# Performance work log

Measured on AMD Instinct MI355X. Metric: run time of the kernel, lower is better.

The kernel has to match this reference:

```python
import jax, jax.numpy as jnp
import numpy as np

D_MODEL = 512
NHEAD = 8
HEAD_DIM = D_MODEL // NHEAD  # 64, also rotary_dim
WIN_LO, WIN_HI = 127, 128    # attn_window: kv in [q-127, q+128]
BLOCK = 256                  # block size for banded attention (>= WIN_LO+1 and >= WIN_HI)


def setup_inputs() -> dict:
    key = jax.random.key(0)
    k1, k2, k3, k4 = jax.random.split(key, 4)
    N, T = 4, 2048
    x = jax.random.normal(k1, (N, T, D_MODEL), dtype=jnp.float32)
    Wqkv_w = jax.random.normal(k2, (3 * D_MODEL, D_MODEL), dtype=jnp.float32) * 0.02
    out_w = jax.random.normal(k3, (D_MODEL, D_MODEL), dtype=jnp.float32) * 0.02
    out_b = jax.random.normal(k4, (D_MODEL,), dtype=jnp.float32) * 0.02
    return {"x": x, "Wqkv_w": Wqkv_w, "out_w": out_w, "out_b": out_b}


def _rotate_half(u):
    u1, u2 = jnp.split(u, 2, axis=-1)
    return jnp.concatenate((-u2, u1), axis=-1)


def _apply_rope(q, k, T, dtype):
    # inv_freq: [HEAD_DIM/2]
    inv_freq = 1.0 / (10000.0 ** (jnp.arange(0, HEAD_DIM, 2, dtype=jnp.float32) / HEAD_DIM))
    pos = jnp.arange(T, dtype=dtype)
    freqs = pos[:, None] * inv_freq[None, :].astype(dtype)      # [T, D/2]
    emb = jnp.concatenate((freqs, freqs), axis=-1)              # [T, D]
    cos = jnp.cos(emb)[None, :, None, :]                        # [1,T,1,D]
    sin = jnp.sin(emb)[None, :, None, :]
    q = q * cos + _rotate_half(q) * sin
    k = k * cos + _rotate_half(k) * sin
    return q, k


def reference(x, Wqkv_w, out_w, out_b):
    N, T, dm = x.shape
    H, D, B = NHEAD, HEAD_DIM, BLOCK
    qkv = (x @ Wqkv_w.T).reshape(N, T, 3, H, D)
    q, k, v = qkv[:, :, 0], qkv[:, :, 1], qkv[:, :, 2]          # [N,T,H,D]
    q, k = _apply_rope(q, k, T, x.dtype)
    # [N,H,T,D]
    q = q.transpose(0, 2, 1, 3)
    k = k.transpose(0, 2, 1, 3)
    v = v.transpose(0, 2, 1, 3)

    nb = T // B
    qb = q.reshape(N, H, nb, B, D)
    kb = k.reshape(N, H, nb, B, D)
    vb = v.reshape(N, H, nb, B, D)
    # pad one block of zeros on each side so block g sees key blocks g-1,g,g+1
    pad = ((0, 0), (0, 0), (1, 1), (0, 0), (0, 0))
    kp = jnp.pad(kb, pad)
    vp = jnp.pad(vb, pad)
    # [N,H,nb,3B,D]
    kwin = jnp.concatenate([kp[:, :, i:i + nb] for i in range(3)], axis=3)
    vwin = jnp.concatenate([vp[:, :, i:i + nb] for i in range(3)], axis=3)

    scale = 1.0 / np.sqrt(D)
    scores = jnp.einsum('nhgqd,nhgkd->nhgqk', qb, kwin) * scale  # [N,H,nb,B,3B]

    qi = jnp.arange(B)
    kj = jnp.arange(3 * B)
    gidx = jnp.arange(nb)
    diff = kj[None, None, :] - B - qi[None, :, None]             # [1,B,3B] kv - q offset
    band = (diff >= -WIN_LO) & (diff <= WIN_HI)
    kv_global = gidx[:, None, None] * B + kj[None, None, :] - B  # [nb,1,3B]
    valid = (kv_global >= 0) & (kv_global < T)
    mask = band & valid                                          # [nb,B,3B]

    neg = jnp.asarray(-1e30, dtype=scores.dtype)
    scores = jnp.where(mask[None, None], scores, neg)
    probs = jax.nn.softmax(scores, axis=-1)
    attn = jnp.einsum('nhgqk,nhgkd->nhgqd', probs, vwin)         # [N,H,nb,B,D]
    attn = attn.reshape(N, H, T, D).transpose(0, 2, 1, 3).reshape(N, T, dm)
    return attn @ out_w.T + out_b
```

## Files before the change

kernel.cpp:

```cpp
#include <hip/hip_runtime.h>
#include <math.h>


typedef __attribute__((ext_vector_type(8))) __bf16 bf16x8;
typedef __attribute__((ext_vector_type(4))) float f32x4;

__device__ __forceinline__ unsigned short f2bf(float f) {
    unsigned int u = __float_as_uint(f);
    u += 0x7fffu + ((u >> 16) & 1u);
    return (unsigned short)(u >> 16);
}
__device__ __forceinline__ unsigned int packbf2(float a, float b) {
    unsigned int ua = __float_as_uint(a); ua += 0x7fffu + ((ua >> 16) & 1u);
    unsigned int ub = __float_as_uint(b); ub += 0x7fffu + ((ub >> 16) & 1u);
    return (ua >> 16) | (ub & 0xffff0000u);
}
__device__ __forceinline__ bf16x8 as_bf16x8(uint4 u) {
    union { uint4 u4; bf16x8 v; } c; c.u4 = u; return c.v;
}
__device__ __forceinline__ bf16x8 ld_frag(const unsigned short* p) {
    return as_bf16x8(*(const uint4*)p);
}

__device__ __forceinline__ void async16(void* lds, const void* g) {
    __builtin_amdgcn_global_load_lds(
        (const __attribute__((address_space(1))) void*)g,
        (__attribute__((address_space(3))) void*)lds,
        16, 0, 0);
}

__global__ __launch_bounds__(256) void cvt_all(
    const float* __restrict__ x, const float* __restrict__ w1,
    const float* __restrict__ w2,
    unsigned short* __restrict__ xb, unsigned short* __restrict__ w1b,
    unsigned short* __restrict__ w2b)
{
    const int n_x  = 8192 * 512 / 4;
    const int n_w1 = 1536 * 512 / 4;
    const int n_w2 = 512 * 512 / 4;
    int i = blockIdx.x * 256 + threadIdx.x;
    const float* in; unsigned short* out; int j;
    if (i < n_x)                    { in = x;  out = xb;  j = i; }
    else if (i < n_x + n_w1)        { in = w1; out = w1b; j = i - n_x; }
    else if (i < n_x + n_w1 + n_w2) { in = w2; out = w2b; j = i - n_x - n_w1; }
    else return;
    float4 v = *(const float4*)(in + 4 * (size_t)j);
    uint2 o;
    o.x = packbf2(v.x, v.y);
    o.y = packbf2(v.z, v.w);
    *(uint2*)(out + 4 * (size_t)j) = o;
}

__global__ __launch_bounds__(256) void gemm_bt_mfma(
    const unsigned short* __restrict__ A, const unsigned short* __restrict__ B,
    const float* __restrict__ bias, void* __restrict__ Cout,
    int M, int O, int K, int write_bf16, int do_rope)
{
    __shared__ __align__(16) unsigned short As[128 * 64];
    __shared__ __align__(16) unsigned short Bs[64 * 64];

    const int tid  = threadIdx.x;
    const int wave = tid >> 6;
    const int lane = tid & 63;
    const int l15  = lane & 15;
    const int lg   = lane >> 4;
    const int row0 = blockIdx.x * 128;
    const int col0 = blockIdx.y * 64;
    const int wr   = wave * 32;

    f32x4 acc[2][4] = {};

    const int srow = tid >> 3;
    const int skg  = ((tid & 7) * 8) ^ ((srow & 7) * 8);

    const int fx = (l15 & 7) * 8;

    for (int k0 = 0; k0 < K; k0 += 64) {
        #pragma unroll
        for (int s = 0; s < 4; ++s)
            async16(&As[(size_t)(s * 256 + tid) * 8],
                    A + (size_t)(row0 + s * 32 + srow) * K + k0 + skg);
        #pragma unroll
        for (int s = 0; s < 2; ++s)
            async16(&Bs[(size_t)(s * 256 + tid) * 8],
                    B + (size_t)(col0 + s * 32 + srow) * K + k0 + skg);
        __syncthreads();

        #pragma unroll
        for (int kstep = 0; kstep < 2; ++kstep) {
            const int kq = (kstep * 32 + lg * 8) ^ fx;
            bf16x8 af[2], bfr[4];
            #pragma unroll
            for (int mt = 0; mt < 2; ++mt)
                af[mt] = ld_frag(&As[(wr + mt * 16 + l15) * 64 + kq]);
            #pragma unroll
            for (int nt = 0; nt < 4; ++nt)
                bfr[nt] = ld_frag(&Bs[(nt * 16 + l15) * 64 + kq]);
            #pragma unroll
            for (int mt = 0; mt < 2; ++mt)
                #pragma unroll
                for (int nt = 0; nt < 4; ++nt)
                    acc[mt][nt] = __builtin_amdgcn_mfma_f32_16x16x32_bf16(
                        af[mt], bfr[nt], acc[mt][nt], 0, 0, 0);
        }
        __syncthreads();
    }

    const int qrow = lg * 4;

    if (do_rope && col0 < 1024) {
        const float cfreq = 0.28782313662425574f;
        const float invf0 = __expf(-(float)l15 * cfreq);
        const float invf1 = __expf(-(float)(16 + l15) * cfreq);
        #pragma unroll
        for (int mt = 0; mt < 2; ++mt) {
            #pragma unroll
            for (int r = 0; r < 4; ++r) {
                const int t = (row0 + wr + mt * 16 + qrow + r) & 2047;
                #pragma unroll
                for (int p = 0; p < 2; ++p) {
                    float ang = (float)t * (p ? invf1 : invf0);
                    float s, c;
                    __sincosf(ang, &s, &c);
                    float a = acc[mt][p][r];
                    float b = acc[mt][p + 2][r];
                    acc[mt][p][r]     = a * c - b * s;
                    acc[mt][p + 2][r] = b * c + a * s;
                }
            }
        }
        if (col0 < 512) {
            #pragma unroll
            for (int mt = 0; mt < 2; ++mt)
                #pragma unroll
                for (int nt = 0; nt < 4; ++nt)
                    #pragma unroll
                    for (int r = 0; r < 4; ++r)
                        acc[mt][nt][r] *= 0.125f;
        }
    }

    #pragma unroll
    for (int nt = 0; nt < 4; ++nt) {
        const int col = col0 + nt * 16 + l15;
        const float bv = bias ? bias[col] : 0.f;
        #pragma unroll
        for (int mt = 0; mt < 2; ++mt) {
            const int rowb = row0 + wr + mt * 16 + qrow;
            if (write_bf16) {
                unsigned short* C = (unsigned short*)Cout;
                #pragma unroll
                for (int r = 0; r < 4; ++r)
                    C[(size_t)(rowb + r) * O + col] = f2bf(acc[mt][nt][r] + bv);
            } else {
                float* C = (float*)Cout;
                #pragma unroll
                for (int r = 0; r < 4; ++r)
                    C[(size_t)(rowb + r) * O + col] = acc[mt][nt][r] + bv;
            }
        }
    }
}

__global__ __launch_bounds__(256) void attn_mfma_kernel(
    const unsigned short* __restrict__ qkv, unsigned short* __restrict__ attnout)
{
    __shared__ __align__(16) unsigned short Kt[64 * 72];
    __shared__ __align__(16) unsigned short Vt[64 * 72];
    __shared__ __align__(16) unsigned short Ps[4][16 * 72];

    const int qt = blockIdx.x;
    const int h  = blockIdx.y;
    const int n  = blockIdx.z;
    const int t0 = qt * 64;
    const int tid  = threadIdx.x;
    const int wave = tid >> 6;
    const int lane = tid & 63;
    const int l15  = lane & 15;
    const int lg   = lane >> 4;

    const size_t base = (size_t)n * 2048 * 1536 + (size_t)h * 64;

    bf16x8 qfrag[2];
    {
        const unsigned short* qp = qkv + base + (size_t)(t0 + wave * 16 + l15) * 1536;
        qfrag[0] = ld_frag(qp + lg * 8);
        qfrag[1] = ld_frag(qp + 32 + lg * 8);
    }

    const int skey = tid >> 2;
    const int sd0  = (tid & 3) * 16;

    float m_r[4], l_r[4];
    #pragma unroll
    for (int r = 0; r < 4; ++r) { m_r[r] = -1e30f; l_r[r] = 0.f; }
    f32x4 acc_o[4] = {};

    for (int dt = -2; dt <= 2; ++dt) {
        const int kt = qt + dt;
        if (kt < 0 || kt > 31) continue;
        const int s0 = kt * 64;

        {
            const unsigned short* kp = qkv + base + 512 + (size_t)(s0 + skey) * 1536 + sd0;
            uint4 k0 = *(const uint4*)kp;
            uint4 k1 = *(const uint4*)(kp + 8);
            *(uint4*)&Kt[skey * 72 + sd0]     = k0;
            *(uint4*)&Kt[skey * 72 + sd0 + 8] = k1;

            const unsigned short* vp = qkv + base + 1024 + (size_t)(s0 + skey) * 1536 + sd0;
            uint4 a = *(const uint4*)vp;
            uint4 b = *(const uint4*)(vp + 8);
            Vt[(sd0 +  0) * 72 + skey] = (unsigned short)(a.x & 0xffffu);
            Vt[(sd0 +  1) * 72 + skey] = (unsigned short)(a.x >> 16);
            Vt[(sd0 +  2) * 72 + skey] = (unsigned short)(a.y & 0xffffu);
            Vt[(sd0 +  3) * 72 + skey] = (unsigned short)(a.y >> 16);
            Vt[(sd0 +  4) * 72 + skey] = (unsigned short)(a.z & 0xffffu);
            Vt[(sd0 +  5) * 72 + skey] = (unsigned short)(a.z >> 16);
            Vt[(sd0 +  6) * 72 + skey] = (unsigned short)(a.w & 0xffffu);
            Vt[(sd0 +  7) * 72 + skey] = (unsigned short)(a.w >> 16);
            Vt[(sd0 +  8) * 72 + skey] = (unsigned short)(b.x & 0xffffu);
            Vt[(sd0 +  9) * 72 + skey] = (unsigned short)(b.x >> 16);
            Vt[(sd0 + 10) * 72 + skey] = (unsigned short)(b.y & 0xffffu);
            Vt[(sd0 + 11) * 72 + skey] = (unsigned short)(b.y >> 16);
            Vt[(sd0 + 12) * 72 + skey] = (unsigned short)(b.z & 0xffffu);
            Vt[(sd0 + 13) * 72 + skey] = (unsigned short)(b.z >> 16);
            Vt[(sd0 + 14) * 72 + skey] = (unsigned short)(b.w & 0xffffu);
            Vt[(sd0 + 15) * 72 + skey] = (unsigned short)(b.w >> 16);
        }
        __syncthreads();

        f32x4 acc_s[4] = {};
        #pragma unroll
        for (int kstep = 0; kstep < 2; ++kstep) {
            #pragma unroll
            for (int nt = 0; nt < 4; ++nt) {
                bf16x8 kf = ld_frag(&Kt[(nt * 16 + l15) * 72 + kstep * 32 + lg * 8]);
                acc_s[nt] = __builtin_amdgcn_mfma_f32_16x16x32_bf16(
                    qfrag[kstep], kf, acc_s[nt], 0, 0, 0);
            }
        }

        float sc[4][4];
        #pragma unroll
        for (int nt = 0; nt < 4; ++nt) {
            const int key_off = dt * 64 + nt * 16 + l15;
            #pragma unroll
            for (int r = 0; r < 4; ++r) {
                const int diff = key_off - (wave * 16 + lg * 4 + r);
                const bool ok = (diff >= -127) && (diff <= 128);
                sc[nt][r] = ok ? acc_s[nt][r] : -1e30f;
            }
        }
        #pragma unroll
        for (int r = 0; r < 4; ++r) {
            float tm = fmaxf(fmaxf(sc[0][r], sc[1][r]), fmaxf(sc[2][r], sc[3][r]));
            tm = fmaxf(tm, __shfl_xor(tm, 1, 64));
            tm = fmaxf(tm, __shfl_xor(tm, 2, 64));
            tm = fmaxf(tm, __shfl_xor(tm, 4, 64));
            tm = fmaxf(tm, __shfl_xor(tm, 8, 64));
            const float m_new = fmaxf(m_r[r], tm);
            const float alpha = __expf(m_r[r] - m_new);
            float psum = 0.f;
            #pragma unroll
            for (int nt = 0; nt < 4; ++nt) {
                float p = __expf(sc[nt][r] - m_new);
                sc[nt][r] = p;
                psum += p;
            }
            psum += __shfl_xor(psum, 1, 64);
            psum += __shfl_xor(psum, 2, 64);
            psum += __shfl_xor(psum, 4, 64);
            psum += __shfl_xor(psum, 8, 64);
            l_r[r] = l_r[r] * alpha + psum;
            m_r[r] = m_new;
            #pragma unroll
            for (int nt = 0; nt < 4; ++nt) acc_o[nt][r] *= alpha;
        }

        #pragma unroll
        for (int nt = 0; nt < 4; ++nt)
            #pragma unroll
            for (int r = 0; r < 4; ++r)
                Ps[wave][(lg * 4 + r) * 72 + nt * 16 + l15] = f2bf(sc[nt][r]);

        __syncthreads();

        bf16x8 pfrag[2];
        pfrag[0] = ld_frag(&Ps[wave][l15 * 72 + lg * 8]);
        pfrag[1] = ld_frag(&Ps[wave][l15 * 72 + 32 + lg * 8]);

        #pragma unroll
        for (int kstep = 0; kstep < 2; ++kstep) {
            #pragma unroll
            for (int nt = 0; nt < 4; ++nt) {
                bf16x8 vf = ld_frag(&Vt[(nt * 16 + l15) * 72 + kstep * 32 + lg * 8]);
                acc_o[nt] = __builtin_amdgcn_mfma_f32_16x16x32_bf16(
                    pfrag[kstep], vf, acc_o[nt], 0, 0, 0);
            }
        }
        __syncthreads();
    }

    float inv_l[4];
    #pragma unroll
    for (int r = 0; r < 4; ++r) inv_l[r] = 1.0f / l_r[r];

    #pragma unroll
    for (int r = 0; r < 4; ++r) {
        const int tq = t0 + wave * 16 + lg * 4 + r;
        unsigned short* op = attnout + (size_t)(n * 2048 + tq) * 512 + h * 64;
        #pragma unroll
        for (int nt = 0; nt < 4; ++nt)
            op[nt * 16 + l15] = f2bf(acc_o[nt][r] * inv_l[r]);
    }
}

extern "C" void kernel_launch(void* const* d_in, const int* in_sizes, int n_in,
                              void* d_out, int out_size, void* d_ws, size_t ws_size,
                              hipStream_t stream)
{
    (void)in_sizes; (void)n_in; (void)out_size; (void)ws_size;

    const float* x     = (const float*)d_in[0];
    const float* Wqkv  = (const float*)d_in[1];
    const float* out_w = (const float*)d_in[2];
    const float* out_b = (const float*)d_in[3];
    float* out = (float*)d_out;

    unsigned short* qkvb  = (unsigned short*)d_ws;
    unsigned short* attnb = qkvb + (size_t)8192 * 1536;
    unsigned short* xb    = attnb + (size_t)8192 * 512;
    unsigned short* wqkvb = xb + (size_t)8192 * 512;
    unsigned short* outwb = wqkvb + (size_t)1536 * 512;

    cvt_all<<<5120, 256, 0, stream>>>(x, Wqkv, out_w, xb, wqkvb, outwb);

    gemm_bt_mfma<<<dim3(64, 24), 256, 0, stream>>>(xb, wqkvb, nullptr, qkvb,
                                                   8192, 1536, 512, 1, 1);
    attn_mfma_kernel<<<dim3(32, 8, 4), 256, 0, stream>>>(qkvb, attnb);
    gemm_bt_mfma<<<dim3(64, 8), 256, 0, stream>>>(attnb, outwb, out_b, out,
                                                  8192, 512, 512, 0, 0);
}
```

Measured before the change: 136.7 us.

## Fuse fp32-to-bf16 conversion into GEMM loads and skip masked attention tiles

```diff
diff --git a/kernel.cpp b/kernel.cpp
--- a/kernel.cpp
+++ b/kernel.cpp
@@ -21,38 +21,18 @@
 __device__ __forceinline__ bf16x8 ld_frag(const unsigned short* p) {
     return as_bf16x8(*(const uint4*)p);
 }
-
-__device__ __forceinline__ void async16(void* lds, const void* g) {
-    __builtin_amdgcn_global_load_lds(
-        (const __attribute__((address_space(1))) void*)g,
-        (__attribute__((address_space(3))) void*)lds,
-        16, 0, 0);
-}
-
-__global__ __launch_bounds__(256) void cvt_all(
-    const float* __restrict__ x, const float* __restrict__ w1,
-    const float* __restrict__ w2,
-    unsigned short* __restrict__ xb, unsigned short* __restrict__ w1b,
-    unsigned short* __restrict__ w2b)
-{
-    const int n_x  = 8192 * 512 / 4;
-    const int n_w1 = 1536 * 512 / 4;
-    const int n_w2 = 512 * 512 / 4;
-    int i = blockIdx.x * 256 + threadIdx.x;
-    const float* in; unsigned short* out; int j;
-    if (i < n_x)                    { in = x;  out = xb;  j = i; }
-    else if (i < n_x + n_w1)        { in = w1; out = w1b; j = i - n_x; }
-    else if (i < n_x + n_w1 + n_w2) { in = w2; out = w2b; j = i - n_x - n_w1; }
-    else return;
-    float4 v = *(const float4*)(in + 4 * (size_t)j);
-    uint2 o;
-    o.x = packbf2(v.x, v.y);
-    o.y = packbf2(v.z, v.w);
-    *(uint2*)(out + 4 * (size_t)j) = o;
-}
-
+__device__ __forceinline__ uint4 pack8(const float4& a, const float4& b) {
+    uint4 o;
+    o.x = packbf2(a.x, a.y);
+    o.y = packbf2(a.z, a.w);
+    o.z = packbf2(b.x, b.y);
+    o.w = packbf2(b.z, b.w);
+    return o;
+}
+
+template<int AF32, int BF32>
 __global__ __launch_bounds__(256) void gemm_bt_mfma(
-    const unsigned short* __restrict__ A, const unsigned short* __restrict__ B,
+    const void* __restrict__ Av, const void* __restrict__ Bv,
     const float* __restrict__ bias, void* __restrict__ Cout,
     int M, int O, int K, int write_bf16, int do_rope)
 {
@@ -71,19 +51,53 @@
     f32x4 acc[2][4] = {};
 
     const int srow = tid >> 3;
-    const int skg  = ((tid & 7) * 8) ^ ((srow & 7) * 8);
-
-    const int fx = (l15 & 7) * 8;
+    const int ldk  = (tid & 7) * 8;
+    const int skg  = ldk ^ ((srow & 7) * 8);
+    const int fx   = (l15 & 7) * 8;
 
     for (int k0 = 0; k0 < K; k0 += 64) {
+        uint4 a_st[4], b_st[2];
+        if (AF32) {
+            const float* A = (const float*)Av;
+            float4 f[4][2];
+            #pragma unroll
+            for (int s = 0; s < 4; ++s) {
+                const float* p = A + (size_t)(row0 + s * 32 + srow) * K + k0 + skg;
+                f[s][0] = ((const float4*)p)[0];
+                f[s][1] = ((const float4*)p)[1];
+            }
+            #pragma unroll
+            for (int s = 0; s < 4; ++s) a_st[s] = pack8(f[s][0], f[s][1]);
+        } else {
+            const unsigned short* A = (const unsigned short*)Av;
+            #pragma unroll
+            for (int s = 0; s < 4; ++s)
+                a_st[s] = *(const uint4*)(A + (size_t)(row0 + s * 32 + srow) * K + k0 + skg);
+        }
+        if (BF32) {
+            const float* B = (const float*)Bv;
+            float4 f[2][2];
+            #pragma unroll
+            for (int s = 0; s < 2; ++s) {
+                const float* p = B + (size_t)(col0 + s * 32 + srow) * K + k0 + skg;
+                f[s][0] = ((const float4*)p)[0];
+                f[s][1] = ((const float4*)p)[1];
+            }
+            #pragma unroll
+            for (int s = 0; s < 2; ++s) b_st[s] = pack8(f[s][0], f[s][1]);
+        } else {
+            const unsigned short* B = (const unsigned short*)Bv;
+            #pragma unroll
+            for (int s = 0; s < 2; ++s)
+                b_st[s] = *(const uint4*)(B + (size_t)(col0 + s * 32 + srow) * K + k0 + skg);
+        }
+
         #pragma unroll
         for (int s = 0; s < 4; ++s)
-            async16(&As[(size_t)(s * 256 + tid) * 8],
-                    A + (size_t)(row0 + s * 32 + srow) * K + k0 + skg);
+            *(uint4*)&As[(s * 32 + srow) * 64 + ldk] = a_st[s];
         #pragma unroll
         for (int s = 0; s < 2; ++s)
-            async16(&Bs[(size_t)(s * 256 + tid) * 8],
-                    B + (size_t)(col0 + s * 32 + srow) * K + k0 + skg);
+            *(uint4*)&Bs[(s * 32 + srow) * 64 + ldk] = b_st[s];
         __syncthreads();
 
         #pragma unroll
@@ -235,6 +249,7 @@
         for (int kstep = 0; kstep < 2; ++kstep) {
             #pragma unroll
             for (int nt = 0; nt < 4; ++nt) {
+                if ((dt == -2 && nt < wave) || (dt == 2 && nt > wave)) continue;
                 bf16x8 kf = ld_frag(&Kt[(nt * 16 + l15) * 72 + kstep * 32 + lg * 8]);
                 acc_s[nt] = __builtin_amdgcn_mfma_f32_16x16x32_bf16(
                     qfrag[kstep], kf, acc_s[nt], 0, 0, 0);
@@ -330,15 +345,10 @@
 
     unsigned short* qkvb  = (unsigned short*)d_ws;
     unsigned short* attnb = qkvb + (size_t)8192 * 1536;
-    unsigned short* xb    = attnb + (size_t)8192 * 512;
-    unsigned short* wqkvb = xb + (size_t)8192 * 512;
-    unsigned short* outwb = wqkvb + (size_t)1536 * 512;
-
-    cvt_all<<<5120, 256, 0, stream>>>(x, Wqkv, out_w, xb, wqkvb, outwb);
-
-    gemm_bt_mfma<<<dim3(64, 24), 256, 0, stream>>>(xb, wqkvb, nullptr, qkvb,
-                                                   8192, 1536, 512, 1, 1);
+
+    gemm_bt_mfma<1, 1><<<dim3(64, 24), 256, 0, stream>>>(
+        x, Wqkv, nullptr, qkvb, 8192, 1536, 512, 1, 1);
     attn_mfma_kernel<<<dim3(32, 8, 4), 256, 0, stream>>>(qkvb, attnb);
-    gemm_bt_mfma<<<dim3(64, 8), 256, 0, stream>>>(attnb, outwb, out_b, out,
-                                                  8192, 512, 512, 0, 0);
-}
+    gemm_bt_mfma<0, 1><<<dim3(64, 8), 256, 0, stream>>>(
+        attnb, out_w, out_b, out, 8192, 512, 512, 0, 0);
+}
```

Result: slower. 164.0 us (+20.0%).

## Process two query tiles per attention block to reuse K/V tiles and skip masked MFMAs

Applied to the files above, without the earlier changes.

```diff
diff --git a/kernel.cpp b/kernel.cpp
--- a/kernel.cpp
+++ b/kernel.cpp
@@ -72,8 +72,7 @@
 
     const int srow = tid >> 3;
     const int skg  = ((tid & 7) * 8) ^ ((srow & 7) * 8);
-
-    const int fx = (l15 & 7) * 8;
+    const int fx   = (l15 & 7) * 8;
 
     for (int k0 = 0; k0 < K; k0 += 64) {
         #pragma unroll
@@ -167,12 +166,11 @@
 {
     __shared__ __align__(16) unsigned short Kt[64 * 72];
     __shared__ __align__(16) unsigned short Vt[64 * 72];
-    __shared__ __align__(16) unsigned short Ps[4][16 * 72];
-
-    const int qt = blockIdx.x;
+    __shared__ __align__(16) unsigned short Ps[2][4][16 * 72];
+
+    const int qb = blockIdx.x;
     const int h  = blockIdx.y;
     const int n  = blockIdx.z;
-    const int t0 = qt * 64;
     const int tid  = threadIdx.x;
     const int wave = tid >> 6;
     const int lane = tid & 63;
@@ -181,23 +179,28 @@
 
     const size_t base = (size_t)n * 2048 * 1536 + (size_t)h * 64;
 
-    bf16x8 qfrag[2];
-    {
-        const unsigned short* qp = qkv + base + (size_t)(t0 + wave * 16 + l15) * 1536;
-        qfrag[0] = ld_frag(qp + lg * 8);
-        qfrag[1] = ld_frag(qp + 32 + lg * 8);
+    bf16x8 qfrag[2][2];
+    #pragma unroll
+    for (int j = 0; j < 2; ++j) {
+        const int tq = (2 * qb + j) * 64 + wave * 16 + l15;
+        const unsigned short* qp = qkv + base + (size_t)tq * 1536;
+        qfrag[j][0] = ld_frag(qp + lg * 8);
+        qfrag[j][1] = ld_frag(qp + 32 + lg * 8);
     }
 
     const int skey = tid >> 2;
     const int sd0  = (tid & 3) * 16;
 
-    float m_r[4], l_r[4];
-    #pragma unroll
-    for (int r = 0; r < 4; ++r) { m_r[r] = -1e30f; l_r[r] = 0.f; }
-    f32x4 acc_o[4] = {};
-
-    for (int dt = -2; dt <= 2; ++dt) {
-        const int kt = qt + dt;
+    float m_r[2][4], l_r[2][4];
+    #pragma unroll
+    for (int j = 0; j < 2; ++j)
+        #pragma unroll
+        for (int r = 0; r < 4; ++r) { m_r[j][r] = -1e30f; l_r[j][r] = 0.f; }
+    f32x4 acc_o[2][4] = {};
+
+    #pragma unroll
+    for (int kk = 0; kk < 6; ++kk) {
+        const int kt = 2 * qb - 2 + kk;
         if (kt < 0 || kt > 31) continue;
         const int s0 = kt * 64;
 
@@ -230,89 +233,102 @@
         }
         __syncthreads();
 
-        f32x4 acc_s[4] = {};
-        #pragma unroll
-        for (int kstep = 0; kstep < 2; ++kstep) {
+        #pragma unroll
+        for (int j = 0; j < 2; ++j) {
+            const int dt = kk - 2 - j;
+            if (dt < -2 || dt > 2) continue;
+
+            f32x4 acc_s[4] = {};
+            #pragma unroll
+            for (int kstep = 0; kstep < 2; ++kstep) {
+                #pragma unroll
+                for (int nt = 0; nt < 4; ++nt) {
+                    if ((dt == -2 && nt < wave) || (dt == 2 && nt > wave))
+                        continue;
+                    bf16x8 kf = ld_frag(&Kt[(nt * 16 + l15) * 72 + kstep * 32 + lg * 8]);
+                    acc_s[nt] = __builtin_amdgcn_mfma_f32_16x16x32_bf16(
+                        qfrag[j][kstep], kf, acc_s[nt], 0, 0, 0);
+                }
+            }
+
+            float sc[4][4];
             #pragma unroll
             for (int nt = 0; nt < 4; ++nt) {
-                bf16x8 kf = ld_frag(&Kt[(nt * 16 + l15) * 72 + kstep * 32 + lg * 8]);
-                acc_s[nt] = __builtin_amdgcn_mfma_f32_16x16x32_bf16(
-                    qfrag[kstep], kf, acc_s[nt], 0, 0, 0);
-            }
-        }
-
-        float sc[4][4];
-        #pragma unroll
-        for (int nt = 0; nt < 4; ++nt) {
-            const int key_off = dt * 64 + nt * 16 + l15;
+                const int key_off = dt * 64 + nt * 16 + l15;
+                #pragma unroll
+                for (int r = 0; r < 4; ++r) {
+                    const int diff = key_off - (wave * 16 + lg * 4 + r);
+                    const bool ok = (diff >= -127) && (diff <= 128);
+                    sc[nt][r] = ok ? acc_s[nt][r] : -1e30f;
+                }
+            }
             #pragma unroll
             for (int r = 0; r < 4; ++r) {
-                const int diff = key_off - (wave * 16 + lg * 4 + r);
-                const bool ok = (diff >= -127) && (diff <= 128);
-                sc[nt][r] = ok ? acc_s[nt][r] : -1e30f;
-            }
-        }
+                float tm = fmaxf(fmaxf(sc[0][r], sc[1][r]), fmaxf(sc[2][r], sc[3][r]));
+                tm = fmaxf(tm, __shfl_xor(tm, 1, 64));
+                tm = fmaxf(tm, __shfl_xor(tm, 2, 64));
+                tm = fmaxf(tm, __shfl_xor(tm, 4, 64));
+                tm = fmaxf(tm, __shfl_xor(tm, 8, 64));
+                const float m_new = fmaxf(m_r[j][r], tm);
+                const float alpha = __expf(m_r[j][r] - m_new);
+                float psum = 0.f;
+                #pragma unroll
+                for (int nt = 0; nt < 4; ++nt) {
+                    float p = __expf(sc[nt][r] - m_new);
+                    sc[nt][r] = p;
+                    psum += p;
+                }
+                psum += __shfl_xor(psum, 1, 64);
+                psum += __shfl_xor(psum, 2, 64);
+                psum += __shfl_xor(psum, 4, 64);
+                psum += __shfl_xor(psum, 8, 64);
+                l_r[j][r] = l_r[j][r] * alpha + psum;
+                m_r[j][r] = m_new;
+                #pragma unroll
+                for (int nt = 0; nt < 4; ++nt) acc_o[j][nt][r] *= alpha;
+            }
+
+            #pragma unroll
+            for (int nt = 0; nt < 4; ++nt)
+                #pragma unroll
+                for (int r = 0; r < 4; ++r)
+                    Ps[j][wave][(lg * 4 + r) * 72 + nt * 16 + l15] = f2bf(sc[nt][r]);
+        }
+        __syncthreads();
+
+        #pragma unroll
+        for (int j = 0; j < 2; ++j) {
+            const int dt = kk - 2 - j;
+            if (dt < -2 || dt > 2) continue;
+            bf16x8 pfrag[2];
+            pfrag[0] = ld_frag(&Ps[j][wave][l15 * 72 + lg * 8]);
+            pfrag[1] = ld_frag(&Ps[j][wave][l15 * 72 + 32 + lg * 8]);
+            #pragma unroll
+            for (int kstep = 0; kstep < 2; ++kstep) {
+                #pragma unroll
+                for (int nt = 0; nt < 4; ++nt) {
+                    bf16x8 vf = ld_frag(&Vt[(nt * 16 + l15) * 72 + kstep * 32 + lg * 8]);
+                    acc_o[j][nt] = __builtin_amdgcn_mfma_f32_16x16x32_bf16(
+                        pfrag[kstep], vf, acc_o[j][nt], 0, 0, 0);
+                }
+            }
+        }
+        __syncthreads();
+    }
+
+    #pragma unroll
+    for (int j = 0; j < 2; ++j) {
+        float inv_l[4];
+        #pragma unroll
+        for (int r = 0; r < 4; ++r) inv_l[r] = 1.0f / l_r[j][r];
         #pragma unroll
         for (int r = 0; r < 4; ++r) {
-            float tm = fmaxf(fmaxf(sc[0][r], sc[1][r]), fmaxf(sc[2][r], sc[3][r]));
-            tm = fmaxf(tm, __shfl_xor(tm, 1, 64));
-            tm = fmaxf(tm, __shfl_xor(tm, 2, 64));
-            tm = fmaxf(tm, __shfl_xor(tm, 4, 64));
-            tm = fmaxf(tm, __shfl_xor(tm, 8, 64));
-            const float m_new = fmaxf(m_r[r], tm);
-            const float alpha = __expf(m_r[r] - m_new);
-            float psum = 0.f;
-            #pragma unroll
-            for (int nt = 0; nt < 4; ++nt) {
-                float p = __expf(sc[nt][r] - m_new);
-                sc[nt][r] = p;
-                psum += p;
-            }
-            psum += __shfl_xor(psum, 1, 64);
-            psum += __shfl_xor(psum, 2, 64);
-            psum += __shfl_xor(psum, 4, 64);
-            psum += __shfl_xor(psum, 8, 64);
-            l_r[r] = l_r[r] * alpha + psum;
-            m_r[r] = m_new;
-            #pragma unroll
-            for (int nt = 0; nt < 4; ++nt) acc_o[nt][r] *= alpha;
-        }
-
-        #pragma unroll
-        for (int nt = 0; nt < 4; ++nt)
-            #pragma unroll
-            for (int r = 0; r < 4; ++r)
-                Ps[wave][(lg * 4 + r) * 72 + nt * 16 + l15] = f2bf(sc[nt][r]);
-
-        __syncthreads();
-
-        bf16x8 pfrag[2];
-        pfrag[0] = ld_frag(&Ps[wave][l15 * 72 + lg * 8]);
-        pfrag[1] = ld_frag(&Ps[wave][l15 * 72 + 32 + lg * 8]);
-
-        #pragma unroll
-        for (int kstep = 0; kstep < 2; ++kstep) {
-            #pragma unroll
-            for (int nt = 0; nt < 4; ++nt) {
-                bf16x8 vf = ld_frag(&Vt[(nt * 16 + l15) * 72 + kstep * 32 + lg * 8]);
-                acc_o[nt] = __builtin_amdgcn_mfma_f32_16x16x32_bf16(
-                    pfrag[kstep], vf, acc_o[nt], 0, 0, 0);
-            }
-        }
-        __syncthreads();
-    }
-
-    float inv_l[4];
-    #pragma unroll
-    for (int r = 0; r < 4; ++r) inv_l[r] = 1.0f / l_r[r];
-
-    #pragma unroll
-    for (int r = 0; r < 4; ++r) {
-        const int tq = t0 + wave * 16 + lg * 4 + r;
-        unsigned short* op = attnout + (size_t)(n * 2048 + tq) * 512 + h * 64;
-        #pragma unroll
-        for (int nt = 0; nt < 4; ++nt)
-            op[nt * 16 + l15] = f2bf(acc_o[nt][r] * inv_l[r]);
+            const int tq = (2 * qb + j) * 64 + wave * 16 + lg * 4 + r;
+            unsigned short* op = attnout + (size_t)(n * 2048 + tq) * 512 + h * 64;
+            #pragma unroll
+            for (int nt = 0; nt < 4; ++nt)
+                op[nt * 16 + l15] = f2bf(acc_o[j][nt][r] * inv_l[r]);
+        }
     }
 }
 
@@ -338,7 +354,7 @@
 
     gemm_bt_mfma<<<dim3(64, 24), 256, 0, stream>>>(xb, wqkvb, nullptr, qkvb,
                                                    8192, 1536, 512, 1, 1);
-    attn_mfma_kernel<<<dim3(32, 8, 4), 256, 0, stream>>>(qkvb, attnb);
+    attn_mfma_kernel<<<dim3(16, 8, 4), 256, 0, stream>>>(qkvb, attnb);
     gemm_bt_mfma<<<dim3(64, 8), 256, 0, stream>>>(attnb, outwb, out_b, out,
                                                   8192, 512, 512, 0, 0);
 }
```

Measured after the change: 139.1 us. No clear change (+1.8%).
